# Performance work log

Hardware: AMD Instinct MI355X
Metric: run time of the kernel (lower is better)

The kernel has to match this reference:

```python
import jax, jax.numpy as jnp
import numpy as np

B, S, D, E, K = 4, 4096, 2048, 64, 2

def setup_inputs() -> dict:
    key = jax.random.key(0)
    kx, kw = jax.random.split(key)
    x = jax.random.normal(kx, (B, S, D), dtype=jnp.float32)
    W = jax.random.normal(kw, (E, D), dtype=jnp.float32) * (1.0 / np.sqrt(D))
    b = jnp.zeros((E,), dtype=jnp.float32)
    return {"x": x, "W": W, "b": b, "k": K}

def reference(x, W, b, k):
    # logits: [B, S, E]
    logits = jnp.einsum('bsd,ed->bse', x, W) + b
    probs = jax.nn.softmax(logits, axis=-1)
    topk_probs, topk_experts = jax.lax.top_k(probs, k)  # [B,S,k]
    # one-hot over experts, OR-reduce over k -> bool mask [B,S,E]
    onehot = jax.nn.one_hot(topk_experts, E, dtype=jnp.int32)  # [B,S,k,E]
    masks = onehot.sum(axis=-2).astype(jnp.bool_)
    return (masks, probs)
```

## Files before the change

### kernel.cpp

```cpp
#include <hip/hip_runtime.h>
#include <math.h>

#define NTOK    16384
#define DDIM    2048
#define NEXP    64
#define PSTRIDE (NTOK * NEXP)
#define KP      128
#define NPH     16
#define PLANE_H 8192
#define SLICE_B 32768

#define AS1 __attribute__((address_space(1)))
#define AS3 __attribute__((address_space(3)))

typedef _Float16 half8   __attribute__((ext_vector_type(8)));
typedef float    floatx4 __attribute__((ext_vector_type(4)));

__global__ __launch_bounds__(256) void wconv_kernel(
    const float* __restrict__ W, _Float16* __restrict__ ws)
{
    const int g     = blockIdx.x * 256 + threadIdx.x;
    const int p     = g >> 11;
    const int L     = g & 2047;
    const int plane = L >> 10;
    const int e     = (L >> 4) & 63;
    const int cp    = L & 15;
    const int c     = cp ^ (e & 7);
    const int k     = (p << 7) + (c << 3);

    const float* src = &W[(size_t)e * DDIM + k];
    floatx4 w0 = *(const floatx4*)src;
    floatx4 w1 = *(const floatx4*)(src + 4);

    half8 o;
#pragma unroll
    for (int i = 0; i < 4; ++i) {
        float f0 = w0[i], f1 = w1[i];
        _Float16 h0 = (_Float16)f0, h1 = (_Float16)f1;
        if (plane == 0) { o[i] = h0; o[4 + i] = h1; }
        else {
            o[i]     = (_Float16)((f0 - (float)h0) * 2048.0f);
            o[4 + i] = (_Float16)((f1 - (float)h1) * 2048.0f);
        }
    }
    *(half8*)((char*)ws + (size_t)g * 16) = o;
}

__global__ __launch_bounds__(256, 2) void router_kernel(
    const float* __restrict__ x,
    const _Float16* __restrict__ ws,
    const float* __restrict__ bias,
    float* __restrict__ out)
{
    __shared__ _Float16 lds[2][SLICE_B / 2];

    const int tid  = threadIdx.x;
    const int lane = tid & 63;
    const int wid  = tid >> 6;
    const int t    = wid >> 1;
    const int h    = wid & 1;
    const int t0   = blockIdx.x * 32 + t * 16;
    const int mrow = lane & 15;
    const int quad = lane >> 4;

    floatx4 acc_hh[4], acc_md[4];
#pragma unroll
    for (int j = 0; j < 4; ++j) { acc_hh[j] = (floatx4)0.0f; acc_md[j] = (floatx4)0.0f; }

    const float* xrow = x + (size_t)(t0 + mrow) * DDIM + h * 64 + quad * 8;

    const char* gslice0 = (const char*)ws;
    char*       lbase[2] = { (char*)&lds[0][0] + wid * 8192,
                             (char*)&lds[1][0] + wid * 8192 };

#define STAGE(P, BUF)                                                          \
    {                                                                          \
        const char* gsrc = gslice0 + (size_t)(P) * SLICE_B + wid * 8192 + lane * 16; \
        char*       ldst = lbase[BUF];                                         \
        _Pragma("unroll")                                                      \
        for (int i = 0; i < 8; ++i)                                            \
            __builtin_amdgcn_global_load_lds(                                  \
                (const AS1 unsigned int*)(const void*)(gsrc + i * 1024),       \
                (AS3 unsigned int*)(void*)(ldst + i * 1024), 16, 0, 0);        \
    }

    floatx4 xc[4], xn[4];

    STAGE(0, 0);
#pragma unroll
    for (int s = 0; s < 2; ++s) {
        xc[2 * s]     = *(const floatx4*)(xrow + s * 32);
        xc[2 * s + 1] = *(const floatx4*)(xrow + s * 32 + 4);
    }
    __syncthreads();

#pragma unroll 2
    for (int p = 0; p < NPH; ++p) {
        if (p < NPH - 1) {
            STAGE(p + 1, (p + 1) & 1);
            const float* xp = xrow + (p + 1) * KP;
#pragma unroll
            for (int s = 0; s < 2; ++s) {
                xn[2 * s]     = *(const floatx4*)(xp + s * 32);
                xn[2 * s + 1] = *(const floatx4*)(xp + s * 32 + 4);
            }
        }

        const _Float16* lb = &lds[p & 1][0];
#pragma unroll
        for (int s = 0; s < 2; ++s) {
            half8 a_hi, a_lo;
#pragma unroll
            for (int i = 0; i < 4; ++i) {
                float fv = xc[2 * s][i];
                _Float16 hh = (_Float16)fv;
                a_hi[i] = hh;
                a_lo[i] = (_Float16)((fv - (float)hh) * 2048.0f);
            }
#pragma unroll
            for (int i = 0; i < 4; ++i) {
                float fv = xc[2 * s + 1][i];
                _Float16 hh = (_Float16)fv;
                a_hi[4 + i] = hh;
                a_lo[4 + i] = (_Float16)((fv - (float)hh) * 2048.0f);
            }
#pragma unroll
            for (int j = 0; j < 4; ++j) {
                const int e   = j * 16 + mrow;
                const int c   = h * 8 + s * 4 + quad;
                const int off = e * 128 + ((c ^ (e & 7)) << 3);
                half8 bh = *(const half8*)(lb + off);
                half8 bl = *(const half8*)(lb + PLANE_H + off);
                acc_hh[j] = __builtin_amdgcn_mfma_f32_16x16x32_f16(a_hi, bh, acc_hh[j], 0, 0, 0);
                acc_md[j] = __builtin_amdgcn_mfma_f32_16x16x32_f16(a_hi, bl, acc_md[j], 0, 0, 0);
                acc_md[j] = __builtin_amdgcn_mfma_f32_16x16x32_f16(a_lo, bh, acc_md[j], 0, 0, 0);
            }
        }

        if (p < NPH - 1) {
#pragma unroll
            for (int i = 0; i < 4; ++i) xc[i] = xn[i];
        }
        __syncthreads();
    }

    float lg[4][4];
#pragma unroll
    for (int j = 0; j < 4; ++j)
#pragma unroll
        for (int r = 0; r < 4; ++r)
            lg[j][r] = acc_hh[j][r] + acc_md[j][r] * (1.0f / 2048.0f);

    float* rbuf = (float*)&lds[0][0];
    if (h == 1) {
#pragma unroll
        for (int j = 0; j < 4; ++j)
#pragma unroll
            for (int r = 0; r < 4; ++r)
                rbuf[t * 1024 + (j * 4 + r) * 64 + lane] = lg[j][r];
    }
    __syncthreads();
    if (h == 1) return;

#pragma unroll
    for (int j = 0; j < 4; ++j) {
        const float bj = bias[j * 16 + mrow];
#pragma unroll
        for (int r = 0; r < 4; ++r)
            lg[j][r] += rbuf[t * 1024 + (j * 4 + r) * 64 + lane] + bj;
    }

    const int c = mrow;
#pragma unroll
    for (int r = 0; r < 4; ++r) {
        const int trow = t0 + quad * 4 + r;

        float m = lg[0][r];
#pragma unroll
        for (int j = 1; j < 4; ++j) m = fmaxf(m, lg[j][r]);
#pragma unroll
        for (int off = 1; off <= 8; off <<= 1) m = fmaxf(m, __shfl_xor(m, off));

        float pj[4], s = 0.0f;
#pragma unroll
        for (int j = 0; j < 4; ++j) { pj[j] = __expf(lg[j][r] - m); s += pj[j]; }
#pragma unroll
        for (int off = 1; off <= 8; off <<= 1) s += __shfl_xor(s, off);
        const float rinv = 1.0f / s;

        float v1 = -1e30f, v2 = -1e30f; int i1 = -1, i2 = -1;
#pragma unroll
        for (int j = 0; j < 4; ++j) {
            float v = lg[j][r]; int e = j * 16 + c;
            if (v > v1 || (v == v1 && e < i1)) { v2 = v1; i2 = i1; v1 = v; i1 = e; }
            else if (v > v2 || (v == v2 && e < i2)) { v2 = v; i2 = e; }
        }
#pragma unroll
        for (int off = 1; off <= 8; off <<= 1) {
            float u1 = __shfl_xor(v1, off); int q1 = __shfl_xor(i1, off);
            float u2 = __shfl_xor(v2, off); int q2 = __shfl_xor(i2, off);
            if (u1 > v1 || (u1 == v1 && q1 < i1)) {
                if (v1 > u2 || (v1 == u2 && i1 < q2)) { v2 = v1; i2 = i1; }
                else                                   { v2 = u2; i2 = q2; }
                v1 = u1; i1 = q1;
            } else {
                if (u1 > v2 || (u1 == v2 && q1 < i2)) { v2 = u1; i2 = q1; }
            }
        }

#pragma unroll
        for (int j = 0; j < 4; ++j) {
            const int col = j * 16 + c;
            const size_t o = (size_t)trow * NEXP + col;
            out[o]           = (col == i1 || col == i2) ? 1.0f : 0.0f;
            out[PSTRIDE + o] = pj[j] * rinv;
        }
    }
}

extern "C" void kernel_launch(void* const* d_in, const int* in_sizes, int n_in,
                              void* d_out, int out_size, void* d_ws, size_t ws_size,
                              hipStream_t stream) {
    const float* x = (const float*)d_in[0];
    const float* W = (const float*)d_in[1];
    const float* b = (const float*)d_in[2];
    (void)in_sizes; (void)n_in; (void)out_size; (void)ws_size;
    float* out = (float*)d_out;

    _Float16* ws = (_Float16*)d_ws;

    hipLaunchKernelGGL(wconv_kernel, dim3(128), dim3(256), 0, stream, W, ws);
    hipLaunchKernelGGL(router_kernel, dim3(NTOK / 32), dim3(256), 0, stream, x, ws, b, out);
}
```

Baseline: 200.3 us.

## Give each wave a private LDS double buffer and split K across wave halves

```diff
diff --git a/kernel.cpp b/kernel.cpp
--- a/kernel.cpp
+++ b/kernel.cpp
@@ -5,10 +5,8 @@
 #define DDIM    2048
 #define NEXP    64
 #define PSTRIDE (NTOK * NEXP)
-#define KP      128
-#define NPH     16
-#define PLANE_H 8192
-#define SLICE_B 32768
+#define ITERS   32
+#define SLICE_B 8192
 
 #define AS1 __attribute__((address_space(1)))
 #define AS3 __attribute__((address_space(3)))
@@ -20,13 +18,14 @@
     const float* __restrict__ W, _Float16* __restrict__ ws)
 {
     const int g     = blockIdx.x * 256 + threadIdx.x;
-    const int p     = g >> 11;
-    const int L     = g & 2047;
-    const int plane = L >> 10;
-    const int e     = (L >> 4) & 63;
-    const int cp    = L & 15;
-    const int c     = cp ^ (e & 7);
-    const int k     = (p << 7) + (c << 3);
+    const int i32   = g >> 9;
+    const int L     = g & 511;
+    const int plane = L >> 8;
+    const int r     = L & 255;
+    const int e     = r >> 2;
+    const int cp    = r & 3;
+    const int c     = cp ^ ((e >> 1) & 3);
+    const int k     = (i32 << 5) + (c << 3);
 
     const float* src = &W[(size_t)e * DDIM + k];
     floatx4 w0 = *(const floatx4*)src;
@@ -52,7 +51,7 @@
     const float* __restrict__ bias,
     float* __restrict__ out)
 {
-    __shared__ _Float16 lds[2][SLICE_B / 2];
+    __shared__ __align__(16) char wlds[4][2][SLICE_B];
 
     const int tid  = threadIdx.x;
     const int lane = tid & 63;
@@ -67,81 +66,70 @@
 #pragma unroll
     for (int j = 0; j < 4; ++j) { acc_hh[j] = (floatx4)0.0f; acc_md[j] = (floatx4)0.0f; }
 
-    const float* xrow = x + (size_t)(t0 + mrow) * DDIM + h * 64 + quad * 8;
-
-    const char* gslice0 = (const char*)ws;
-    char*       lbase[2] = { (char*)&lds[0][0] + wid * 8192,
-                             (char*)&lds[1][0] + wid * 8192 };
-
-#define STAGE(P, BUF)                                                          \
+    const float* xrow = x + (size_t)(t0 + mrow) * DDIM + h * 1024 + quad * 8;
+    const char* wsrc = (const char*)ws + (size_t)h * 32 * SLICE_B + lane * 16;
+    char* buf0 = &wlds[wid][0][0];
+    char* buf1 = &wlds[wid][1][0];
+
+    int boff[4];
+#pragma unroll
+    for (int j = 0; j < 4; ++j) {
+        const int e = j * 16 + mrow;
+        boff[j] = e * 32 + ((quad ^ ((e >> 1) & 3)) << 3);
+    }
+
+#define DMA_SLICE(I, DST)                                                      \
     {                                                                          \
-        const char* gsrc = gslice0 + (size_t)(P) * SLICE_B + wid * 8192 + lane * 16; \
-        char*       ldst = lbase[BUF];                                         \
+        const char* gs = wsrc + (size_t)(I) * SLICE_B;                         \
         _Pragma("unroll")                                                      \
-        for (int i = 0; i < 8; ++i)                                            \
+        for (int q = 0; q < 8; ++q)                                            \
             __builtin_amdgcn_global_load_lds(                                  \
-                (const AS1 unsigned int*)(const void*)(gsrc + i * 1024),       \
-                (AS3 unsigned int*)(void*)(ldst + i * 1024), 16, 0, 0);        \
-    }
-
-    floatx4 xc[4], xn[4];
-
-    STAGE(0, 0);
-#pragma unroll
-    for (int s = 0; s < 2; ++s) {
-        xc[2 * s]     = *(const floatx4*)(xrow + s * 32);
-        xc[2 * s + 1] = *(const floatx4*)(xrow + s * 32 + 4);
-    }
-    __syncthreads();
+                (const AS1 unsigned int*)(const void*)(gs + q * 1024),         \
+                (AS3 unsigned int*)(void*)((DST) + q * 1024), 16, 0, 0);       \
+    }
+
+    DMA_SLICE(0, buf0);
+    floatx4 xa0 = *(const floatx4*)(xrow);
+    floatx4 xa1 = *(const floatx4*)(xrow + 4);
+    floatx4 xb0 = *(const floatx4*)(xrow + 32);
+    floatx4 xb1 = *(const floatx4*)(xrow + 36);
 
 #pragma unroll 2
-    for (int p = 0; p < NPH; ++p) {
-        if (p < NPH - 1) {
-            STAGE(p + 1, (p + 1) & 1);
-            const float* xp = xrow + (p + 1) * KP;
-#pragma unroll
-            for (int s = 0; s < 2; ++s) {
-                xn[2 * s]     = *(const floatx4*)(xp + s * 32);
-                xn[2 * s + 1] = *(const floatx4*)(xp + s * 32 + 4);
-            }
-        }
-
-        const _Float16* lb = &lds[p & 1][0];
-#pragma unroll
-        for (int s = 0; s < 2; ++s) {
-            half8 a_hi, a_lo;
-#pragma unroll
-            for (int i = 0; i < 4; ++i) {
-                float fv = xc[2 * s][i];
-                _Float16 hh = (_Float16)fv;
-                a_hi[i] = hh;
-                a_lo[i] = (_Float16)((fv - (float)hh) * 2048.0f);
-            }
-#pragma unroll
-            for (int i = 0; i < 4; ++i) {
-                float fv = xc[2 * s + 1][i];
-                _Float16 hh = (_Float16)fv;
-                a_hi[4 + i] = hh;
-                a_lo[4 + i] = (_Float16)((fv - (float)hh) * 2048.0f);
-            }
-#pragma unroll
-            for (int j = 0; j < 4; ++j) {
-                const int e   = j * 16 + mrow;
-                const int c   = h * 8 + s * 4 + quad;
-                const int off = e * 128 + ((c ^ (e & 7)) << 3);
-                half8 bh = *(const half8*)(lb + off);
-                half8 bl = *(const half8*)(lb + PLANE_H + off);
-                acc_hh[j] = __builtin_amdgcn_mfma_f32_16x16x32_f16(a_hi, bh, acc_hh[j], 0, 0, 0);
-                acc_md[j] = __builtin_amdgcn_mfma_f32_16x16x32_f16(a_hi, bl, acc_md[j], 0, 0, 0);
-                acc_md[j] = __builtin_amdgcn_mfma_f32_16x16x32_f16(a_lo, bh, acc_md[j], 0, 0, 0);
-            }
-        }
-
-        if (p < NPH - 1) {
-#pragma unroll
-            for (int i = 0; i < 4; ++i) xc[i] = xn[i];
-        }
-        __syncthreads();
+    for (int i = 0; i < ITERS; ++i) {
+        if (i + 1 < ITERS) DMA_SLICE(i + 1, (i & 1) ? buf0 : buf1);
+        floatx4 xn0, xn1;
+        if (i + 2 < ITERS) {
+            xn0 = *(const floatx4*)(xrow + (i + 2) * 32);
+            xn1 = *(const floatx4*)(xrow + (i + 2) * 32 + 4);
+        }
+
+        half8 a_hi, a_lo;
+#pragma unroll
+        for (int q = 0; q < 4; ++q) {
+            float fv = xa0[q];
+            _Float16 hh = (_Float16)fv;
+            a_hi[q] = hh;
+            a_lo[q] = (_Float16)((fv - (float)hh) * 2048.0f);
+        }
+#pragma unroll
+        for (int q = 0; q < 4; ++q) {
+            float fv = xa1[q];
+            _Float16 hh = (_Float16)fv;
+            a_hi[4 + q] = hh;
+            a_lo[4 + q] = (_Float16)((fv - (float)hh) * 2048.0f);
+        }
+
+        const _Float16* lb = (const _Float16*)((i & 1) ? buf1 : buf0);
+#pragma unroll
+        for (int j = 0; j < 4; ++j) {
+            half8 bh = *(const half8*)(lb + boff[j]);
+            half8 bl = *(const half8*)(lb + 2048 + boff[j]);
+            acc_hh[j] = __builtin_amdgcn_mfma_f32_16x16x32_f16(a_hi, bh, acc_hh[j], 0, 0, 0);
+            acc_md[j] = __builtin_amdgcn_mfma_f32_16x16x32_f16(a_hi, bl, acc_md[j], 0, 0, 0);
+            acc_md[j] = __builtin_amdgcn_mfma_f32_16x16x32_f16(a_lo, bh, acc_md[j], 0, 0, 0);
+        }
+
+        xa0 = xb0; xa1 = xb1; xb0 = xn0; xb1 = xn1;
     }
 
     float lg[4][4];
@@ -151,7 +139,8 @@
         for (int r = 0; r < 4; ++r)
             lg[j][r] = acc_hh[j][r] + acc_md[j][r] * (1.0f / 2048.0f);
 
-    float* rbuf = (float*)&lds[0][0];
+    __syncthreads();
+    float* rbuf = (float*)&wlds[0][0][0];
     if (h == 1) {
 #pragma unroll
         for (int j = 0; j < 4; ++j)
```

Result: slower. 225.8 us (+12.7%).
